# Performance work log

Hardware: AMD Instinct MI355X
Metric: run time of the kernel (lower is better)

The kernel has to match this reference:

```python
import jax, jax.numpy as jnp
import numpy as np

N = 8192        # particles
NBH = 64        # black holes
L = 46.0        # box side -> ~32 neighbors per particle at radius 4.5
K = 4           # kernel_size per axis
KK = K * K * K
EXTENT = 9.0    # radius_scale(1.5) * 6 * particle_radius(1)
EXTENT_BH = 4.0 * EXTENT
EP = 300000     # padded particle-particle edge count
EB = 160000     # padded bh->particle edge count
CIN = 4         # vel(3) + mass(1)
C0, C1, C2, C3 = 32, 64, 64, 3
FOUR_OVER_PI = 4.0 / np.pi


def _ball_query_np(query, points, radius, cap, pad_seg):
    """Brute-force host-side ball query. Returns padded (src, dst); padding
    uses dst == pad_seg (a sentinel segment that is dropped later)."""
    r2 = radius * radius
    src, dst = [], []
    for i in range(0, query.shape[0], 1024):
        q = query[i:i + 1024]
        d2 = ((q[:, None, :] - points[None, :, :]) ** 2).sum(-1)
        m = (d2 < r2) & (d2 > 0.0)  # radius_search_ignore_query_points
        qi, pj = np.nonzero(m)
        dst.append(qi + i)
        src.append(pj)
    src = np.concatenate(src).astype(np.int32)
    dst = np.concatenate(dst).astype(np.int32)
    n = min(len(src), cap)
    out_s = np.zeros(cap, np.int32)
    out_d = np.full(cap, pad_seg, np.int32)
    out_s[:n] = src[:n]
    out_d[:n] = dst[:n]
    return out_s, out_d


def setup_inputs() -> dict:
    rng = np.random.RandomState(0)
    pos = (rng.rand(N, 3) * L).astype(np.float32)
    vel = rng.randn(N, 3).astype(np.float32)
    mass = rng.rand(N).astype(np.float32)
    bh_pos = (rng.rand(NBH, 3) * L).astype(np.float32)
    bh_vel = rng.randn(NBH, 3).astype(np.float32)
    bh_mass = (rng.rand(NBH) * 10.0).astype(np.float32)
    pp_src, pp_dst = _ball_query_np(pos, pos, EXTENT * 0.5, EP, N)
    bh_src, bh_dst = _ball_query_np(pos, bh_pos, EXTENT_BH * 0.5, EB, N)

    def w(*s):
        return (rng.randn(*s) * 0.05).astype(np.float32)

    inp = dict(
        pos=jnp.asarray(pos), vel=jnp.asarray(vel), mass=jnp.asarray(mass),
        bh_pos=jnp.asarray(bh_pos), bh_vel=jnp.asarray(bh_vel), bh_mass=jnp.asarray(bh_mass),
        pp_src=jnp.asarray(pp_src), pp_dst=jnp.asarray(pp_dst),
        bh_src=jnp.asarray(bh_src), bh_dst=jnp.asarray(bh_dst),
        W0a=jnp.asarray(w(K, K, K, CIN, C0)), b0a=jnp.zeros(C0, jnp.float32),
        Wd0=jnp.asarray(w(CIN, C0)), bd0=jnp.zeros(C0, jnp.float32),
        W0b=jnp.asarray(w(K, K, K, CIN, C0)), b0b=jnp.zeros(C0, jnp.float32),
        W1=jnp.asarray(w(K, K, K, 3 * C0, C1)), b1=jnp.zeros(C1, jnp.float32),
        Wd1=jnp.asarray(w(3 * C0, C1)), bd1=jnp.zeros(C1, jnp.float32),
        W2=jnp.asarray(w(K, K, K, C1, C2)), b2=jnp.zeros(C2, jnp.float32),
        Wd2=jnp.asarray(w(C1, C2)), bd2=jnp.zeros(C2, jnp.float32),
        W3=jnp.asarray(w(K, K, K, C2, C3)), b3=jnp.zeros(C3, jnp.float32),
        Wd3=jnp.asarray(w(C2, C3)), bd3=jnp.zeros(C3, jnp.float32),
    )
    return inp


def _ball_to_cube(p):
    """Volume-preserving map from unit ball to cube [-1,1]^3 (sphere->cylinder->cube)."""
    eps = 1e-8
    x, y, z = p[..., 0], p[..., 1], p[..., 2]
    sq = x * x + y * y + z * z
    nrm = jnp.sqrt(sq)
    xy = x * x + y * y
    # sphere -> cylinder
    caps = 1.25 * z * z > xy
    s_caps = jnp.sqrt(3.0 * nrm / (nrm + jnp.abs(z) + eps))
    s_side = nrm / jnp.sqrt(xy + eps)
    s = jnp.where(caps, s_caps, s_side)
    valid = sq > eps
    cx = jnp.where(valid, x * s, 0.0)
    cy = jnp.where(valid, y * s, 0.0)
    cz = jnp.where(valid, jnp.where(caps, jnp.sign(z) * nrm, 1.5 * z), 0.0)
    # cylinder -> cube (concentric disc-to-square, area preserving)
    rxy = jnp.sqrt(cx * cx + cy * cy)
    regA = cx * cx >= cy * cy
    safe_cx = jnp.where(jnp.abs(cx) > eps, cx, 1.0)
    safe_cy = jnp.where(jnp.abs(cy) > eps, cy, 1.0)
    uA = jnp.sign(cx) * rxy
    vA = uA * FOUR_OVER_PI * jnp.arctan(cy / safe_cx)
    vB = jnp.sign(cy) * rxy
    uB = vB * FOUR_OVER_PI * jnp.arctan(cx / safe_cy)
    okxy = rxy > eps
    u = jnp.where(okxy, jnp.where(regA, uA, uB), 0.0)
    v = jnp.where(okxy, jnp.where(regA, vA, vB), 0.0)
    return jnp.stack([u, v, cz], axis=-1)


def _cconv(feats, pos_src, pos_dst, src, dst, W, b, extent):
    """ContinuousConv: ball-query edges (src->dst), poly6 window, trilinear
    kernel interpolation (align_corners=True), scatter-sum, no normalization."""
    n_out = pos_dst.shape[0]
    radius = 0.5 * extent
    ps = jnp.take(pos_src, src, axis=0)                       # [E,3]
    pd = jnp.take(pos_dst, jnp.minimum(dst, n_out - 1), axis=0)
    d = (ps - pd) * (1.0 / radius)                            # normalized offsets
    r_sqr = jnp.sum(d * d, axis=-1)
    win = jnp.clip((1.0 - r_sqr) ** 3, 0.0, 1.0)              # window_poly6
    u = _ball_to_cube(d)                                      # in [-1,1]^3
    t = (u + 1.0) * (0.5 * (K - 1))                           # align_corners grid coords
    i0f = jnp.clip(jnp.floor(t), 0, K - 2)
    i0 = i0f.astype(jnp.int32)
    f = t - i0f                                               # trilinear fractions
    fe = jnp.take(feats, src, axis=0) * win[:, None]          # [E,Cin]
    Cin = feats.shape[1]
    Wf = W.reshape(KK, Cin, -1)
    T = jnp.zeros(((n_out + 1) * KK, Cin), feats.dtype)
    for dx in (0, 1):
        wx = f[:, 0] if dx else 1.0 - f[:, 0]
        for dy in (0, 1):
            wy = f[:, 1] if dy else 1.0 - f[:, 1]
            for dz in (0, 1):
                wz = f[:, 2] if dz else 1.0 - f[:, 2]
                k = ((i0[:, 0] + dx) * K + (i0[:, 1] + dy)) * K + (i0[:, 2] + dz)
                idx = dst * KK + k                            # sentinel dst==n_out dropped
                T = T + jax.ops.segment_sum((wx * wy * wz)[:, None] * fe, idx,
                                            num_segments=(n_out + 1) * KK)
    T = T.reshape(n_out + 1, KK, Cin)[:n_out]                 # [N,64,Cin]
    return jnp.einsum('nkc,kcd->nd', T, Wf) + b


def _forward(pos, vel, mass, bh_pos, bh_vel, bh_mass,
             W0a, b0a, Wd0, bd0, W0b, b0b, W1, b1, Wd1, bd1,
             W2, b2, Wd2, bd2, W3, b3, Wd3, bd3,
             pp_src, pp_dst, bh_src, bh_dst):
    feats = jnp.concatenate([vel, mass[:, None]], axis=-1)        # [N,4]
    bh_feats = jnp.concatenate([bh_vel, bh_mass[:, None]], axis=-1)
    c0 = _cconv(feats, pos, pos, pp_src, pp_dst, W0a, b0a, EXTENT)      # [N,32]
    d0 = feats @ Wd0 + bd0                                               # [N,32]
    cb = _cconv(bh_feats, bh_pos, pos, bh_src, bh_dst, W0b, b0b, EXTENT_BH)
    h = jnp.concatenate([c0, cb, d0], axis=-1)                           # [N,96]
    c1 = jax.nn.relu(_cconv(h, pos, pos, pp_src, pp_dst, W1, b1, EXTENT))
    d1 = jax.nn.relu(h @ Wd1 + bd1)
    h1 = c1 + d1                                                         # 64 != 96 -> no residual
    c2 = jax.nn.relu(_cconv(h1, pos, pos, pp_src, pp_dst, W2, b2, EXTENT))
    d2 = jax.nn.relu(h1 @ Wd2 + bd2)
    h2 = c2 + d2 + h1                                                    # 64 == 64 -> residual
    c3 = _cconv(h2, pos, pos, pp_src, pp_dst, W3, b3, EXTENT)
    d3 = h2 @ Wd3 + bd3
    return c3 + d3                                                       # accelerations [N,3]


def reference(pos, vel, mass, bh_pos, bh_vel, bh_mass,
              pp_src, pp_dst, bh_src, bh_dst,
              W0a, b0a, Wd0, bd0, W0b, b0b, W1, b1, Wd1, bd1,
              W2, b2, Wd2, bd2, W3, b3, Wd3, bd3):
    return _forward(pos, vel, mass, bh_pos, bh_vel, bh_mass,
                    W0a, b0a, Wd0, bd0, W0b, b0b, W1, b1, Wd1, bd1,
                    W2, b2, Wd2, bd2, W3, b3, Wd3, bd3,
                    pp_src, pp_dst, bh_src, bh_dst)
```

## Files before the change

### kernel.cpp

```cpp
#include <hip/hip_runtime.h>
#include <math.h>

#define NPART 8192
#define NBHX  64
#define EPX   300000
#define EBX   160000
#define FOUR_OVER_PI 1.27323954473516f

typedef __attribute__((ext_vector_type(8))) short bf16x8;
typedef __attribute__((ext_vector_type(4))) float f32x4;

__device__ __forceinline__ float signf(float x){ return (x>0.f)?1.f:((x<0.f)?-1.f:0.f); }
__device__ __forceinline__ unsigned short f2bf(float f){
  unsigned u = __float_as_uint(f);
  u += 0x7FFFu + ((u >> 16) & 1u);
  return (unsigned short)(u >> 16);
}
__device__ __forceinline__ float bf2f(unsigned short h){
  return __uint_as_float(((unsigned)h) << 16);
}
__device__ __forceinline__ float bfl(unsigned u){ return __uint_as_float(u << 16); }
__device__ __forceinline__ float bfh(unsigned u){ return __uint_as_float(u & 0xffff0000u); }

__global__ void feats_kernel(const float* __restrict__ vel, const float* __restrict__ mass,
                             const float* __restrict__ bhvel, const float* __restrict__ bhmass,
                             float* __restrict__ feats, float* __restrict__ bhfeats,
                             int* __restrict__ hist) {
  int i = blockIdx.x*256 + threadIdx.x;
  if (i < NPART) {
    feats[i*4+0]=vel[i*3+0]; feats[i*4+1]=vel[i*3+1]; feats[i*4+2]=vel[i*3+2]; feats[i*4+3]=mass[i];
  }
  if (i < NBHX) {
    bhfeats[i*4+0]=bhvel[i*3+0]; bhfeats[i*4+1]=bhvel[i*3+1]; bhfeats[i*4+2]=bhvel[i*3+2]; bhfeats[i*4+3]=bhmass[i];
  }
  if (i < 4096) hist[i] = 0;
}

__global__ void geom_kernel(const float* __restrict__ ppos, const float* __restrict__ qpos,
                            const int* __restrict__ src, const int* __restrict__ dst,
                            int E, int n_out, float inv_radius,
                            int* __restrict__ gsb, float* __restrict__ gw) {
  int e = blockIdx.x*256 + threadIdx.x;
  if (e >= E) return;
  int s = src[e], t = dst[e];
  if (t >= n_out) {
    gsb[e] = s*64;
    for (int j=0;j<8;j++) gw[(size_t)e*8+j] = 0.f;
    return;
  }
  float x = (ppos[s*3+0] - qpos[t*3+0]) * inv_radius;
  float y = (ppos[s*3+1] - qpos[t*3+1]) * inv_radius;
  float z = (ppos[s*3+2] - qpos[t*3+2]) * inv_radius;
  float r2 = x*x + y*y + z*z;
  float w1 = 1.f - r2;
  float win = fminf(fmaxf(w1*w1*w1, 0.f), 1.f);
  const float eps = 1e-8f;
  float nrm = sqrtf(r2);
  float xy = x*x + y*y;
  bool caps = (1.25f*z*z > xy);
  float s_caps = sqrtf(3.f*nrm/(nrm + fabsf(z) + eps));
  float s_side = nrm / sqrtf(xy + eps);
  float sc = caps ? s_caps : s_side;
  bool valid = r2 > eps;
  float cx = valid ? x*sc : 0.f;
  float cy = valid ? y*sc : 0.f;
  float cz = valid ? (caps ? signf(z)*nrm : 1.5f*z) : 0.f;
  float rxy = sqrtf(cx*cx + cy*cy);
  bool regA = (cx*cx >= cy*cy);
  float safe_cx = (fabsf(cx) > eps) ? cx : 1.0f;
  float safe_cy = (fabsf(cy) > eps) ? cy : 1.0f;
  float uA = signf(cx)*rxy;
  float vA = uA * FOUR_OVER_PI * atanf(cy/safe_cx);
  float vB = signf(cy)*rxy;
  float uB = vB * FOUR_OVER_PI * atanf(cx/safe_cy);
  bool okxy = rxy > eps;
  float u = okxy ? (regA ? uA : uB) : 0.f;
  float v = okxy ? (regA ? vA : vB) : 0.f;
  float tt[3] = { (u+1.f)*1.5f, (v+1.f)*1.5f, (cz+1.f)*1.5f };
  int i0[3]; float f[3];
#pragma unroll
  for (int ax=0; ax<3; ax++) {
    float tf = floorf(tt[ax]);
    tf = fminf(fmaxf(tf, 0.f), 2.f);
    i0[ax] = (int)tf;
    f[ax] = tt[ax] - tf;
  }
  gsb[e] = s*64 + ((i0[0]*4 + i0[1])*4 + i0[2]);
#pragma unroll
  for (int j=0;j<8;j++) {
    float wx = (j&4) ? f[0] : 1.f - f[0];
    float wy = (j&2) ? f[1] : 1.f - f[1];
    float wz = (j&1) ? f[2] : 1.f - f[2];
    gw[(size_t)e*8+j] = win * wx * wy * wz;
  }
}

__global__ void csr2_kernel(const int* __restrict__ dstP, const int* __restrict__ dstB,
                            int* __restrict__ rsP, int* __restrict__ rsB) {
  int i = blockIdx.x*256 + threadIdx.x;
  if (i <= NPART) {
    int lo = 0, hi = EPX;
    while (lo < hi) { int mid = (lo+hi)>>1; if (dstP[mid] < i) lo = mid+1; else hi = mid; }
    rsP[i] = lo;
  }
  int k = i - (NPART+1);
  if (k >= 0 && k <= NPART) {
    int lo = 0, hi = EBX;
    while (lo < hi) { int mid = (lo+hi)>>1; if (dstB[mid] < k) lo = mid+1; else hi = mid; }
    rsB[k] = lo;
  }
}

__global__ void cellhist_kernel(const float* __restrict__ pos, int* __restrict__ cell,
                                int* __restrict__ hist) {
  int i = blockIdx.x*256 + threadIdx.x;
  if (i >= NPART) return;
  const float inv = 16.0f/46.0f;
  int ix = min(15, max(0, (int)(pos[i*3+0]*inv)));
  int iy = min(15, max(0, (int)(pos[i*3+1]*inv)));
  int iz = min(15, max(0, (int)(pos[i*3+2]*inv)));
  int c = (ix*16+iy)*16+iz;
  cell[i] = c;
  atomicAdd(&hist[c], 1);
}
__global__ __launch_bounds__(256) void scan_kernel(const int* __restrict__ hist, int* __restrict__ offs) {
  __shared__ int wsum[4];
  int t = threadIdx.x;
  int base = t*16;
  int loc[16]; int s = 0;
#pragma unroll
  for (int i=0;i<16;i++){ loc[i]=s; s+=hist[base+i]; }
  int lane = t & 63, wv = t >> 6;
  int pre = s;
  for (int off=1; off<64; off<<=1) {
    int v = __shfl_up(pre, off);
    if (lane >= off) pre += v;
  }
  if (lane == 63) wsum[wv] = pre;
  __syncthreads();
  int wbase = 0;
  for (int w=0; w<wv; w++) wbase += wsum[w];
  int ex = wbase + pre - s;
#pragma unroll
  for (int i=0;i<16;i++) offs[base+i] = ex + loc[i];
}
__global__ void scatterorder_kernel(const int* __restrict__ cell, int* __restrict__ offs,
                                    int* __restrict__ order) {
  int i = blockIdx.x*256 + threadIdx.x;
  if (i >= NPART) return;
  int p = atomicAdd(&offs[cell[i]], 1);
  order[p] = i;
}

__device__ __forceinline__ int swz_block(int bid, int nb) {
  return (bid & 7)*(nb >> 3) + (bid >> 3);
}

__global__ void wtrans3_kernel(const float* __restrict__ W1, const float* __restrict__ W2,
                               const float* __restrict__ W3,
                               unsigned short* __restrict__ BT1, unsigned short* __restrict__ BT2,
                               unsigned short* __restrict__ BT3) {
  int idx = blockIdx.x*256 + threadIdx.x;
  const int S1 = 4096*96, S2 = 4096*64, S3 = 256*64;
  if (idx < S1) {
    int n = idx/96, c = idx - n*96; int k = n>>6, d = n&63;
    BT1[idx] = f2bf(W1[((size_t)k*96 + c)*64 + d]);
  } else if (idx < S1+S2) {
    int t = idx - S1; int n = t>>6, c = t&63; int k = n>>6, d = n&63;
    BT2[t] = f2bf(W2[((size_t)k*64 + c)*64 + d]);
  } else if (idx < S1+S2+S3) {
    int t = idx - S1 - S2; int n = t>>6, c = t&63; int k = n>>2, d = n&3;
    BT3[t] = f2bf((d < 3) ? W3[((size_t)k*64 + c)*3 + d] : 0.f);
  }
}

__global__ void y0_kernel(const float* __restrict__ feats4, const float* __restrict__ bhfeats,
                          const float* __restrict__ W0a, const float* __restrict__ W0b,
                          unsigned short* __restrict__ Y0a, unsigned short* __restrict__ Y0b) {
  int idx = blockIdx.x*256 + threadIdx.x;
  if (idx >= (NPART+NBHX)*256) return;
  int oct = idx & 3, k = (idx>>2) & 63, s = idx >> 8;
  bool bh = (s >= NPART);
  int sl = bh ? s - NPART : s;
  const float* fp = (bh ? bhfeats : feats4) + (size_t)sl*4;
  const float* W0 = bh ? W0b : W0a;
  unsigned short* Y = (bh ? Y0b : Y0a) + ((size_t)sl*64 + k)*32 + oct*8;
  float4 f = *(const float4*)fp;
  const float* w = W0 + (size_t)k*128 + oct*8;
  unsigned short o[8];
#pragma unroll
  for (int i=0;i<8;i++) {
    float v = f.x*w[i] + f.y*w[32+i] + f.z*w[64+i] + f.w*w[96+i];
    o[i] = f2bf(v);
  }
  uint4 u;
  u.x = (unsigned)o[0] | ((unsigned)o[1]<<16);
  u.y = (unsigned)o[2] | ((unsigned)o[3]<<16);
  u.z = (unsigned)o[4] | ((unsigned)o[5]<<16);
  u.w = (unsigned)o[6] | ((unsigned)o[7]<<16);
  *(uint4*)Y = u;
}

__global__ __launch_bounds__(256) void gemm_y_kernel(
    const unsigned short* __restrict__ A, const unsigned short* __restrict__ BT,
    int KC, int Ntot, unsigned short* __restrict__ Y) {
  const int wid  = threadIdx.x >> 6;
  const int lane = threadIdx.x & 63;
  const int r = lane & 15, g = lane >> 4;
  const int m0 = blockIdx.x*128 + wid*32;
  const int n0 = blockIdx.y*64;
  f32x4 acc[2][4];
#pragma unroll
  for (int h=0;h<2;h++)
#pragma unroll
    for (int n=0;n<4;n++) acc[h][n] = (f32x4){0.f,0.f,0.f,0.f};
  const unsigned short* A0 = A + (size_t)(m0 + r)*KC;
  const unsigned short* A1 = A + (size_t)(m0 + 16 + r)*KC;
  for (int k0 = 0; k0 < KC; k0 += 32) {
    int ko = k0 + g*8;
    bf16x8 a0 = *(const bf16x8*)(A0 + ko);
    bf16x8 a1 = *(const bf16x8*)(A1 + ko);
#pragma unroll
    for (int n=0; n<4; n++) {
      bf16x8 b = *(const bf16x8*)(BT + (size_t)(n0 + n*16 + r)*KC + ko);
      acc[0][n] = __builtin_amdgcn_mfma_f32_16x16x32_bf16(a0, b, acc[0][n], 0, 0, 0);
      acc[1][n] = __builtin_amdgcn_mfma_f32_16x16x32_bf16(a1, b, acc[1][n], 0, 0, 0);
    }
  }
#pragma unroll
  for (int h=0;h<2;h++)
#pragma unroll
    for (int n=0;n<4;n++)
#pragma unroll
      for (int j=0;j<4;j++)
        Y[(size_t)(m0 + h*16 + g*4 + j)*Ntot + n0 + n*16 + r] = f2bf(acc[h][n][j]);
}

__device__ __forceinline__ void xor_add4(f32x4& a, int mask) {
  a.x += __shfl_xor(a.x, mask);
  a.y += __shfl_xor(a.y, mask);
  a.z += __shfl_xor(a.z, mask);
  a.w += __shfl_xor(a.w, mask);
}

__global__ __launch_bounds__(256) void gather_l0_kernel(
    const int* __restrict__ order,
    const int* __restrict__ rsP, const int* __restrict__ gsbP, const float* __restrict__ gwP,
    const int* __restrict__ rsB, const int* __restrict__ gsbB, const float* __restrict__ gwB,
    const unsigned short* __restrict__ Y0a, const unsigned short* __restrict__ Y0b,
    const float* __restrict__ feats4, const float* __restrict__ Wd0, const float* __restrict__ bd0,
    const float* __restrict__ b0a, const float* __restrict__ b0b,
    float* __restrict__ hf, unsigned short* __restrict__ hb) {
  const int sw = swz_block(blockIdx.x, gridDim.x);
  const int node = order[sw*4 + (threadIdx.x >> 6)];
  const int lane = threadIdx.x & 63;
  const int j = lane >> 3, cg = lane & 7;
  const int koff = ((j&4)<<2) | ((j&2)<<1) | (j&1);
  f32x4 accP = {0.f,0.f,0.f,0.f}, accB = {0.f,0.f,0.f,0.f};
  {
    int e0 = rsP[node], e1 = rsP[node+1];
    int e = e0;
    for (; e + 4 <= e1; e += 4) {
      uint2 y[4]; float w[4];
#pragma unroll
      for (int i=0;i<4;i++) {
        int sb = gsbP[e+i];
        y[i] = *(const uint2*)(Y0a + ((size_t)(sb + koff))*32 + cg*4);
        w[i] = gwP[(size_t)(e+i)*8 + j];
      }
#pragma unroll
      for (int i=0;i<4;i++) {
        accP.x += w[i]*bfl(y[i].x); accP.y += w[i]*bfh(y[i].x);
        accP.z += w[i]*bfl(y[i].y); accP.w += w[i]*bfh(y[i].y);
      }
    }
    for (; e < e1; e++) {
      int sb = gsbP[e];
      uint2 y = *(const uint2*)(Y0a + ((size_t)(sb + koff))*32 + cg*4);
      float w = gwP[(size_t)e*8 + j];
      accP.x += w*bfl(y.x); accP.y += w*bfh(y.x);
      accP.z += w*bfl(y.y); accP.w += w*bfh(y.y);
    }
  }
  {
    int e0 = rsB[node], e1 = rsB[node+1];
    int e = e0;
    for (; e + 4 <= e1; e += 4) {
      uint2 y[4]; float w[4];
#pragma unroll
      for (int i=0;i<4;i++) {
        int sb = gsbB[e+i];
        y[i] = *(const uint2*)(Y0b + ((size_t)(sb + koff))*32 + cg*4);
        w[i] = gwB[(size_t)(e+i)*8 + j];
      }
#pragma unroll
      for (int i=0;i<4;i++) {
        accB.x += w[i]*bfl(y[i].x); accB.y += w[i]*bfh(y[i].x);
        accB.z += w[i]*bfl(y[i].y); accB.w += w[i]*bfh(y[i].y);
      }
    }
    for (; e < e1; e++) {
      int sb = gsbB[e];
      uint2 y = *(const uint2*)(Y0b + ((size_t)(sb + koff))*32 + cg*4);
      float w = gwB[(size_t)e*8 + j];
      accB.x += w*bfl(y.x); accB.y += w*bfh(y.x);
      accB.z += w*bfl(y.y); accB.w += w*bfh(y.y);
    }
  }
  xor_add4(accP, 8);  xor_add4(accP, 16); xor_add4(accP, 32);
  xor_add4(accB, 8);  xor_add4(accB, 16); xor_add4(accB, 32);
  if (lane < 8) {
    float4 f = *(const float4*)(feats4 + (size_t)node*4);
    float4 ba = *(const float4*)(b0a + cg*4);
    float4 bb = *(const float4*)(b0b + cg*4);
    float4 bdv = *(const float4*)(bd0 + cg*4);
    float4 w0v = *(const float4*)(Wd0 + 0*32 + cg*4);
    float4 w1v = *(const float4*)(Wd0 + 1*32 + cg*4);
    float4 w2v = *(const float4*)(Wd0 + 2*32 + cg*4);
    float4 w3v = *(const float4*)(Wd0 + 3*32 + cg*4);
    float4 dd;
    dd.x = bdv.x + f.x*w0v.x + f.y*w1v.x + f.z*w2v.x + f.w*w3v.x;
    dd.y = bdv.y + f.x*w0v.y + f.y*w1v.y + f.z*w2v.y + f.w*w3v.y;
    dd.z = bdv.z + f.x*w0v.z + f.y*w1v.z + f.z*w2v.z + f.w*w3v.z;
    dd.w = bdv.w + f.x*w0v.w + f.y*w1v.w + f.z*w2v.w + f.w*w3v.w;
    float4 c0; c0.x = accP.x + ba.x; c0.y = accP.y + ba.y; c0.z = accP.z + ba.z; c0.w = accP.w + ba.w;
    float4 cb; cb.x = accB.x + bb.x; cb.y = accB.y + bb.y; cb.z = accB.z + bb.z; cb.w = accB.w + bb.w;
    size_t o = (size_t)node*96;
    *(float4*)(hf + o + cg*4)      = c0;
    *(float4*)(hf + o + 32 + cg*4) = cb;
    *(float4*)(hf + o + 64 + cg*4) = dd;
    ushort4 u0 = {f2bf(c0.x), f2bf(c0.y), f2bf(c0.z), f2bf(c0.w)};
    ushort4 u1 = {f2bf(cb.x), f2bf(cb.y), f2bf(cb.z), f2bf(cb.w)};
    ushort4 u2 = {f2bf(dd.x), f2bf(dd.y), f2bf(dd.z), f2bf(dd.w)};
    *(ushort4*)(hb + o + cg*4)      = u0;
    *(ushort4*)(hb + o + 32 + cg*4) = u1;
    *(ushort4*)(hb + o + 64 + cg*4) = u2;
  }
}

template<int DCIN, bool ADDSKIP>
__global__ __launch_bounds__(128) void gather64_kernel(
    const int* __restrict__ order,
    const int* __restrict__ rs, const int* __restrict__ gsb, const float* __restrict__ gw,
    const unsigned short* __restrict__ Y,
    const float* __restrict__ Xf, const float* __restrict__ Wd, const float* __restrict__ bd,
    const float* __restrict__ bconv, const float* __restrict__ skip,
    float* __restrict__ outf, unsigned short* __restrict__ outb) {
  const int sw = swz_block(blockIdx.x, gridDim.x);
  const int node = order[sw];
  const int wave = threadIdx.x >> 6;
  const int lane = threadIdx.x & 63;
  const int j = lane >> 3, cg = lane & 7;
  const int koff = ((j&4)<<2) | ((j&2)<<1) | (j&1);
  __shared__ __align__(16) float red[64*8];
  f32x4 accA = {0.f,0.f,0.f,0.f}, accB = {0.f,0.f,0.f,0.f};
  const int e0 = rs[node], e1 = rs[node+1];
  int e = e0 + wave;
  for (; e + 6 < e1; e += 8) {
    uint4 y[4]; float w[4];
#pragma unroll
    for (int i=0;i<4;i++) {
      int ee = e + i*2;
      int sb = gsb[ee];
      y[i] = *(const uint4*)(Y + ((size_t)(sb + koff))*64 + cg*8);
      w[i] = gw[(size_t)ee*8 + j];
    }
#pragma unroll
    for (int i=0;i<4;i++) {
      accA.x += w[i]*bfl(y[i].x); accA.y += w[i]*bfh(y[i].x);
      accA.z += w[i]*bfl(y[i].y); accA.w += w[i]*bfh(y[i].y);
      accB.x += w[i]*bfl(y[i].z); accB.y += w[i]*bfh(y[i].z);
      accB.z += w[i]*bfl(y[i].w); accB.w += w[i]*bfh(y[i].w);
    }
  }
  for (; e < e1; e += 2) {
    int sb = gsb[e];
    uint4 y = *(const uint4*)(Y + ((size_t)(sb + koff))*64 + cg*8);
    float w = gw[(size_t)e*8 + j];
    accA.x += w*bfl(y.x); accA.y += w*bfh(y.x);
    accA.z += w*bfl(y.y); accA.w += w*bfh(y.y);
    accB.x += w*bfl(y.z); accB.y += w*bfh(y.z);
    accB.z += w*bfl(y.w); accB.w += w*bfh(y.w);
  }
  if (wave == 1) {
    *(f32x4*)(red + lane*8)     = accA;
    *(f32x4*)(red + lane*8 + 4) = accB;
  }
  __syncthreads();
  if (wave == 0) {
    {
      f32x4 oA = *(const f32x4*)(red + lane*8);
      f32x4 oB = *(const f32x4*)(red + lane*8 + 4);
      accA.x += oA.x; accA.y += oA.y; accA.z += oA.z; accA.w += oA.w;
      accB.x += oB.x; accB.y += oB.y; accB.z += oB.z; accB.w += oB.w;
    }
    constexpr int KQ = DCIN/8;
    f32x4 ddA = {0.f,0.f,0.f,0.f}, ddB = {0.f,0.f,0.f,0.f};
    const float* x = Xf + (size_t)node*DCIN + j*KQ;
#pragma unroll
    for (int kk=0; kk<KQ; kk++) {
      float xv = x[kk];
      float4 w0 = *(const float4*)(Wd + (size_t)(j*KQ+kk)*64 + cg*8);
      float4 w1 = *(const float4*)(Wd + (size_t)(j*KQ+kk)*64 + cg*8 + 4);
      ddA.x += xv*w0.x; ddA.y += xv*w0.y; ddA.z += xv*w0.z; ddA.w += xv*w0.w;
      ddB.x += xv*w1.x; ddB.y += xv*w1.y; ddB.z += xv*w1.z; ddB.w += xv*w1.w;
    }
    xor_add4(accA, 8); xor_add4(accA, 16); xor_add4(accA, 32);
    xor_add4(accB, 8); xor_add4(accB, 16); xor_add4(accB, 32);
    xor_add4(ddA, 8);  xor_add4(ddA, 16);  xor_add4(ddA, 32);
    xor_add4(ddB, 8);  xor_add4(ddB, 16);  xor_add4(ddB, 32);
    if (lane < 8) {
      float4 bc0 = *(const float4*)(bconv + cg*8);
      float4 bc1 = *(const float4*)(bconv + cg*8 + 4);
      float4 bd0v = *(const float4*)(bd + cg*8);
      float4 bd1v = *(const float4*)(bd + cg*8 + 4);
      float4 v0, v1;
      v0.x = fmaxf(accA.x + bc0.x, 0.f) + fmaxf(ddA.x + bd0v.x, 0.f);
      v0.y = fmaxf(accA.y + bc0.y, 0.f) + fmaxf(ddA.y + bd0v.y, 0.f);
      v0.z = fmaxf(accA.z + bc0.z, 0.f) + fmaxf(ddA.z + bd0v.z, 0.f);
      v0.w = fmaxf(accA.w + bc0.w, 0.f) + fmaxf(ddA.w + bd0v.w, 0.f);
      v1.x = fmaxf(accB.x + bc1.x, 0.f) + fmaxf(ddB.x + bd1v.x, 0.f);
      v1.y = fmaxf(accB.y + bc1.y, 0.f) + fmaxf(ddB.y + bd1v.y, 0.f);
      v1.z = fmaxf(accB.z + bc1.z, 0.f) + fmaxf(ddB.z + bd1v.z, 0.f);
      v1.w = fmaxf(accB.w + bc1.w, 0.f) + fmaxf(ddB.w + bd1v.w, 0.f);
      if (ADDSKIP) {
        float4 s0 = *(const float4*)(skip + (size_t)node*64 + cg*8);
        float4 s1 = *(const float4*)(skip + (size_t)node*64 + cg*8 + 4);
        v0.x += s0.x; v0.y += s0.y; v0.z += s0.z; v0.w += s0.w;
        v1.x += s1.x; v1.y += s1.y; v1.z += s1.z; v1.w += s1.w;
      }
      *(float4*)(outf + (size_t)node*64 + cg*8)     = v0;
      *(float4*)(outf + (size_t)node*64 + cg*8 + 4) = v1;
      ushort4 u0 = {f2bf(v0.x), f2bf(v0.y), f2bf(v0.z), f2bf(v0.w)};
      ushort4 u1 = {f2bf(v1.x), f2bf(v1.y), f2bf(v1.z), f2bf(v1.w)};
      *(ushort4*)(outb + (size_t)node*64 + cg*8)     = u0;
      *(ushort4*)(outb + (size_t)node*64 + cg*8 + 4) = u1;
    }
  }
}

__global__ __launch_bounds__(256) void gather3_kernel(
    const int* __restrict__ order,
    const int* __restrict__ rs, const int* __restrict__ gsb, const float* __restrict__ gw,
    const unsigned short* __restrict__ Y3,
    const float* __restrict__ h2f, const float* __restrict__ Wd3, const float* __restrict__ bd3,
    const float* __restrict__ b3, float* __restrict__ out) {
  const int sw = swz_block(blockIdx.x, gridDim.x);
  const int node = order[sw*4 + (threadIdx.x >> 6)];
  const int lane = threadIdx.x & 63;
  const int e2 = lane >> 5, j = (lane >> 2) & 7, dd = lane & 3;
  const int koff = ((j&4)<<2)|((j&2)<<1)|(j&1);
  float acc = 0.f;
  const int e0 = rs[node], e1 = rs[node+1];
  for (int e = e0; e < e1; e += 2) {
    int ee = e + e2;
    bool v = ee < e1;
    int ix = v ? ee : e;
    int sb = gsb[ix];
    float w = v ? gw[(size_t)ix*8 + j] : 0.f;
    acc += w * bf2f(Y3[((size_t)(sb + koff))*4 + dd]);
  }
  acc += __shfl_xor(acc, 4);
  acc += __shfl_xor(acc, 8);
  acc += __shfl_xor(acc, 16);
  acc += __shfl_down(acc, 32);
  if (lane < 3) {
    float d3 = bd3[lane];
    const float* x = h2f + (size_t)node*64;
#pragma unroll 8
    for (int c=0;c<64;c++) d3 += x[c]*Wd3[c*3 + lane];
    out[(size_t)node*3 + lane] = acc + b3[lane] + d3;
  }
}

extern "C" void kernel_launch(void* const* d_in, const int* in_sizes, int n_in,
                              void* d_out, int out_size, void* d_ws, size_t ws_size,
                              hipStream_t stream) {
  const float* pos    = (const float*)d_in[0];
  const float* vel    = (const float*)d_in[1];
  const float* mass   = (const float*)d_in[2];
  const float* bh_pos = (const float*)d_in[3];
  const float* bh_vel = (const float*)d_in[4];
  const float* bh_mass= (const float*)d_in[5];
  const int* pp_src   = (const int*)d_in[6];
  const int* pp_dst   = (const int*)d_in[7];
  const int* bh_src   = (const int*)d_in[8];
  const int* bh_dst   = (const int*)d_in[9];
  const float* W0a=(const float*)d_in[10]; const float* b0a=(const float*)d_in[11];
  const float* Wd0=(const float*)d_in[12]; const float* bd0=(const float*)d_in[13];
  const float* W0b=(const float*)d_in[14]; const float* b0b=(const float*)d_in[15];
  const float* W1 =(const float*)d_in[16]; const float* b1 =(const float*)d_in[17];
  const float* Wd1=(const float*)d_in[18]; const float* bd1=(const float*)d_in[19];
  const float* W2 =(const float*)d_in[20]; const float* b2 =(const float*)d_in[21];
  const float* Wd2=(const float*)d_in[22]; const float* bd2=(const float*)d_in[23];
  const float* W3 =(const float*)d_in[24]; const float* b3 =(const float*)d_in[25];
  const float* Wd3=(const float*)d_in[26]; const float* bd3=(const float*)d_in[27];
  float* out = (float*)d_out;
  char* wsb = (char*)d_ws;

  size_t off = 0;
  auto alloc = [&](size_t nbytes){ size_t o = off; off += (nbytes + 255) & ~((size_t)255); return o; };
  size_t feats_o   = alloc((size_t)NPART*4*4);
  size_t bhfeats_o = alloc((size_t)NBHX*4*4);
  size_t rs_pp_o   = alloc(8256*4);
  size_t rs_bh_o   = alloc(8256*4);
  size_t gsb_pp_o  = alloc((size_t)EPX*4);
  size_t gw_pp_o   = alloc((size_t)EPX*8*4);
  size_t gsb_bh_o  = alloc((size_t)EBX*4);
  size_t gw_bh_o   = alloc((size_t)EBX*8*4);
  size_t hf_o  = alloc((size_t)NPART*96*4);
  size_t hb_o  = alloc((size_t)NPART*96*2);
  size_t h1f_o = alloc((size_t)NPART*64*4);
  size_t h1b_o = alloc((size_t)NPART*64*2);
  size_t h2f_o = alloc((size_t)NPART*64*4);
  size_t h2b_o = alloc((size_t)NPART*64*2);
  size_t bt1_o = alloc((size_t)4096*96*2);
  size_t bt2_o = alloc((size_t)4096*64*2);
  size_t bt3_o = alloc((size_t)256*64*2);
  size_t y0b_o = alloc((size_t)NBHX*64*32*2);
  size_t cell_o = alloc((size_t)NPART*4);
  size_t hist_o = alloc((size_t)4096*4);
  size_t order_o= alloc((size_t)NPART*4);
  size_t y_o   = alloc((size_t)NPART*4096*2);

  float* featsP = (float*)(wsb + feats_o); float* bhfeatsP = (float*)(wsb + bhfeats_o);
  int* rsPP = (int*)(wsb + rs_pp_o); int* rsBH = (int*)(wsb + rs_bh_o);
  int* gsbP = (int*)(wsb + gsb_pp_o); float* gwP = (float*)(wsb + gw_pp_o);
  int* gsbB = (int*)(wsb + gsb_bh_o); float* gwB = (float*)(wsb + gw_bh_o);
  float* hf  = (float*)(wsb + hf_o);  unsigned short* hb  = (unsigned short*)(wsb + hb_o);
  float* h1f = (float*)(wsb + h1f_o); unsigned short* h1b = (unsigned short*)(wsb + h1b_o);
  float* h2f = (float*)(wsb + h2f_o); unsigned short* h2b = (unsigned short*)(wsb + h2b_o);
  unsigned short* BT1 = (unsigned short*)(wsb + bt1_o);
  unsigned short* BT2 = (unsigned short*)(wsb + bt2_o);
  unsigned short* BT3 = (unsigned short*)(wsb + bt3_o);
  unsigned short* Y0b = (unsigned short*)(wsb + y0b_o);
  int* cellA = (int*)(wsb + cell_o);
  int* histA = (int*)(wsb + hist_o);
  int* orderA= (int*)(wsb + order_o);
  unsigned short* Ybuf = (unsigned short*)(wsb + y_o);

  feats_kernel<<<(NPART+255)/256, 256, 0, stream>>>(vel, mass, bh_vel, bh_mass, featsP, bhfeatsP, histA);
  geom_kernel<<<(EPX+255)/256, 256, 0, stream>>>(pos, pos, pp_src, pp_dst, EPX, NPART, 1.f/4.5f, gsbP, gwP);
  geom_kernel<<<(EBX+255)/256, 256, 0, stream>>>(bh_pos, pos, bh_src, bh_dst, EBX, NPART, 1.f/18.f, gsbB, gwB);
  csr2_kernel<<<(2*(NPART+1)+255)/256, 256, 0, stream>>>(pp_dst, bh_dst, rsPP, rsBH);
  cellhist_kernel<<<NPART/256, 256, 0, stream>>>(pos, cellA, histA);
  scan_kernel<<<1, 256, 0, stream>>>(histA, histA);
  scatterorder_kernel<<<NPART/256, 256, 0, stream>>>(cellA, histA, orderA);
  wtrans3_kernel<<<(4096*96 + 4096*64 + 256*64 + 255)/256, 256, 0, stream>>>(W1, W2, W3, BT1, BT2, BT3);

  y0_kernel<<<((NPART+NBHX)*256+255)/256, 256, 0, stream>>>(featsP, bhfeatsP, W0a, W0b, Ybuf, Y0b);
  gather_l0_kernel<<<NPART/4, 256, 0, stream>>>(orderA, rsPP, gsbP, gwP, rsBH, gsbB, gwB,
                                                Ybuf, Y0b, featsP, Wd0, bd0, b0a, b0b, hf, hb);
  {
    dim3 g(NPART/128, 4096/64);
    gemm_y_kernel<<<g, 256, 0, stream>>>(hb, BT1, 96, 4096, Ybuf);
    gather64_kernel<96,false><<<NPART, 128, 0, stream>>>(orderA, rsPP, gsbP, gwP, Ybuf,
        hf, Wd1, bd1, b1, nullptr, h1f, h1b);
  }
  {
    dim3 g(NPART/128, 4096/64);
    gemm_y_kernel<<<g, 256, 0, stream>>>(h1b, BT2, 64, 4096, Ybuf);
    gather64_kernel<64,true><<<NPART, 128, 0, stream>>>(orderA, rsPP, gsbP, gwP, Ybuf,
        h1f, Wd2, bd2, b2, h1f, h2f, h2b);
  }
  {
    dim3 g(NPART/128, 256/64);
    gemm_y_kernel<<<g, 256, 0, stream>>>(h2b, BT3, 64, 256, Ybuf);
    gather3_kernel<<<NPART/4, 256, 0, stream>>>(orderA, rsPP, gsbP, gwP, Ybuf,
        h2f, Wd3, bd3, b3, out);
  }
}
```

Before: 214.8 us.

## Pack per-corner edge index and weight together, merge prep kernels, split dense work

Stores each edge's base index alongside each of its 8 trilinear weights as a uint2 record, so gather kernels fetch index and weight in one load instead of two dependent loads. Merges the geometry kernels for particle and black-hole edges into one launch, folds feature packing into the CSR kernel and cell histogram into the weight transpose kernel. In gather64, the dense-layer dot product is split across both waves and reduced through shared memory. The cost is duplicating the index eight times, which roughly doubles the geometry output bytes, plus a larger shared reduction buffer.

```diff
diff --git a/kernel.cpp b/kernel.cpp
--- a/kernel.cpp
+++ b/kernel.cpp
@@ -22,35 +22,30 @@
 __device__ __forceinline__ float bfl(unsigned u){ return __uint_as_float(u << 16); }
 __device__ __forceinline__ float bfh(unsigned u){ return __uint_as_float(u & 0xffff0000u); }
 
-__global__ void feats_kernel(const float* __restrict__ vel, const float* __restrict__ mass,
-                             const float* __restrict__ bhvel, const float* __restrict__ bhmass,
-                             float* __restrict__ feats, float* __restrict__ bhfeats,
+__global__ void geom2_kernel(const float* __restrict__ pos, const float* __restrict__ bh_pos,
+                             const int* __restrict__ srcP, const int* __restrict__ dstP,
+                             const int* __restrict__ srcB, const int* __restrict__ dstB,
+                             uint2* __restrict__ gewP, uint2* __restrict__ gewB,
                              int* __restrict__ hist) {
-  int i = blockIdx.x*256 + threadIdx.x;
-  if (i < NPART) {
-    feats[i*4+0]=vel[i*3+0]; feats[i*4+1]=vel[i*3+1]; feats[i*4+2]=vel[i*3+2]; feats[i*4+3]=mass[i];
-  }
-  if (i < NBHX) {
-    bhfeats[i*4+0]=bhvel[i*3+0]; bhfeats[i*4+1]=bhvel[i*3+1]; bhfeats[i*4+2]=bhvel[i*3+2]; bhfeats[i*4+3]=bhmass[i];
-  }
-  if (i < 4096) hist[i] = 0;
-}
-
-__global__ void geom_kernel(const float* __restrict__ ppos, const float* __restrict__ qpos,
-                            const int* __restrict__ src, const int* __restrict__ dst,
-                            int E, int n_out, float inv_radius,
-                            int* __restrict__ gsb, float* __restrict__ gw) {
-  int e = blockIdx.x*256 + threadIdx.x;
-  if (e >= E) return;
+  int idx = blockIdx.x*256 + threadIdx.x;
+  if (idx < 4096) hist[idx] = 0;
+  bool isP = idx < EPX;
+  int e = isP ? idx : idx - EPX;
+  if (!isP && e >= EBX) return;
+  const int* src = isP ? srcP : srcB;
+  const int* dst = isP ? dstP : dstB;
+  const float* ppos = isP ? pos : bh_pos;
+  uint2* gew = isP ? gewP : gewB;
+  float inv_radius = isP ? (1.f/4.5f) : (1.f/18.f);
   int s = src[e], t = dst[e];
-  if (t >= n_out) {
-    gsb[e] = s*64;
-    for (int j=0;j<8;j++) gw[(size_t)e*8+j] = 0.f;
+  if (t >= NPART) {
+    uint2 z; z.x = s*64; z.y = 0;
+    for (int j=0;j<8;j++) gew[(size_t)e*8+j] = z;
     return;
   }
-  float x = (ppos[s*3+0] - qpos[t*3+0]) * inv_radius;
-  float y = (ppos[s*3+1] - qpos[t*3+1]) * inv_radius;
-  float z = (ppos[s*3+2] - qpos[t*3+2]) * inv_radius;
+  float x = (ppos[s*3+0] - pos[t*3+0]) * inv_radius;
+  float y = (ppos[s*3+1] - pos[t*3+1]) * inv_radius;
+  float z = (ppos[s*3+2] - pos[t*3+2]) * inv_radius;
   float r2 = x*x + y*y + z*z;
   float w1 = 1.f - r2;
   float win = fminf(fmaxf(w1*w1*w1, 0.f), 1.f);
@@ -85,19 +80,29 @@
     i0[ax] = (int)tf;
     f[ax] = tt[ax] - tf;
   }
-  gsb[e] = s*64 + ((i0[0]*4 + i0[1])*4 + i0[2]);
+  unsigned sb = s*64 + ((i0[0]*4 + i0[1])*4 + i0[2]);
 #pragma unroll
   for (int j=0;j<8;j++) {
     float wx = (j&4) ? f[0] : 1.f - f[0];
     float wy = (j&2) ? f[1] : 1.f - f[1];
     float wz = (j&1) ? f[2] : 1.f - f[2];
-    gw[(size_t)e*8+j] = win * wx * wy * wz;
-  }
-}
-
-__global__ void csr2_kernel(const int* __restrict__ dstP, const int* __restrict__ dstB,
+    uint2 o; o.x = sb; o.y = __float_as_uint(win * wx * wy * wz);
+    gew[(size_t)e*8+j] = o;
+  }
+}
+
+__global__ void prep_kernel(const float* __restrict__ vel, const float* __restrict__ mass,
+                            const float* __restrict__ bhvel, const float* __restrict__ bhmass,
+                            float* __restrict__ feats, float* __restrict__ bhfeats,
+                            const int* __restrict__ dstP, const int* __restrict__ dstB,
                             int* __restrict__ rsP, int* __restrict__ rsB) {
   int i = blockIdx.x*256 + threadIdx.x;
+  if (i < NPART) {
+    feats[i*4+0]=vel[i*3+0]; feats[i*4+1]=vel[i*3+1]; feats[i*4+2]=vel[i*3+2]; feats[i*4+3]=mass[i];
+  }
+  if (i < NBHX) {
+    bhfeats[i*4+0]=bhvel[i*3+0]; bhfeats[i*4+1]=bhvel[i*3+1]; bhfeats[i*4+2]=bhvel[i*3+2]; bhfeats[i*4+3]=bhmass[i];
+  }
   if (i <= NPART) {
     int lo = 0, hi = EPX;
     while (lo < hi) { int mid = (lo+hi)>>1; if (dstP[mid] < i) lo = mid+1; else hi = mid; }
@@ -111,56 +116,25 @@
   }
 }
 
-__global__ void cellhist_kernel(const float* __restrict__ pos, int* __restrict__ cell,
-                                int* __restrict__ hist) {
-  int i = blockIdx.x*256 + threadIdx.x;
-  if (i >= NPART) return;
-  const float inv = 16.0f/46.0f;
-  int ix = min(15, max(0, (int)(pos[i*3+0]*inv)));
-  int iy = min(15, max(0, (int)(pos[i*3+1]*inv)));
-  int iz = min(15, max(0, (int)(pos[i*3+2]*inv)));
-  int c = (ix*16+iy)*16+iz;
-  cell[i] = c;
-  atomicAdd(&hist[c], 1);
-}
-__global__ __launch_bounds__(256) void scan_kernel(const int* __restrict__ hist, int* __restrict__ offs) {
-  __shared__ int wsum[4];
-  int t = threadIdx.x;
-  int base = t*16;
-  int loc[16]; int s = 0;
-#pragma unroll
-  for (int i=0;i<16;i++){ loc[i]=s; s+=hist[base+i]; }
-  int lane = t & 63, wv = t >> 6;
-  int pre = s;
-  for (int off=1; off<64; off<<=1) {
-    int v = __shfl_up(pre, off);
-    if (lane >= off) pre += v;
-  }
-  if (lane == 63) wsum[wv] = pre;
-  __syncthreads();
-  int wbase = 0;
-  for (int w=0; w<wv; w++) wbase += wsum[w];
-  int ex = wbase + pre - s;
-#pragma unroll
-  for (int i=0;i<16;i++) offs[base+i] = ex + loc[i];
-}
-__global__ void scatterorder_kernel(const int* __restrict__ cell, int* __restrict__ offs,
-                                    int* __restrict__ order) {
-  int i = blockIdx.x*256 + threadIdx.x;
-  if (i >= NPART) return;
-  int p = atomicAdd(&offs[cell[i]], 1);
-  order[p] = i;
-}
-
-__device__ __forceinline__ int swz_block(int bid, int nb) {
-  return (bid & 7)*(nb >> 3) + (bid >> 3);
-}
-
-__global__ void wtrans3_kernel(const float* __restrict__ W1, const float* __restrict__ W2,
-                               const float* __restrict__ W3,
-                               unsigned short* __restrict__ BT1, unsigned short* __restrict__ BT2,
-                               unsigned short* __restrict__ BT3) {
-  int idx = blockIdx.x*256 + threadIdx.x;
+__global__ void cellw_kernel(const float* __restrict__ pos, int* __restrict__ cell,
+                             int* __restrict__ hist,
+                             const float* __restrict__ W1, const float* __restrict__ W2,
+                             const float* __restrict__ W3,
+                             unsigned short* __restrict__ BT1, unsigned short* __restrict__ BT2,
+                             unsigned short* __restrict__ BT3) {
+  int b = blockIdx.x;
+  if (b < 32) {
+    int i = b*256 + threadIdx.x;
+    const float inv = 16.0f/46.0f;
+    int ix = min(15, max(0, (int)(pos[i*3+0]*inv)));
+    int iy = min(15, max(0, (int)(pos[i*3+1]*inv)));
+    int iz = min(15, max(0, (int)(pos[i*3+2]*inv)));
+    int c = (ix*16+iy)*16+iz;
+    cell[i] = c;
+    atomicAdd(&hist[c], 1);
+    return;
+  }
+  int idx = (b-32)*256 + threadIdx.x;
   const int S1 = 4096*96, S2 = 4096*64, S3 = 256*64;
   if (idx < S1) {
     int n = idx/96, c = idx - n*96; int k = n>>6, d = n&63;
@@ -172,6 +146,39 @@
     int t = idx - S1 - S2; int n = t>>6, c = t&63; int k = n>>2, d = n&3;
     BT3[t] = f2bf((d < 3) ? W3[((size_t)k*64 + c)*3 + d] : 0.f);
   }
+}
+
+__global__ __launch_bounds__(256) void scan_kernel(const int* __restrict__ hist, int* __restrict__ offs) {
+  __shared__ int wsum[4];
+  int t = threadIdx.x;
+  int base = t*16;
+  int loc[16]; int s = 0;
+#pragma unroll
+  for (int i=0;i<16;i++){ loc[i]=s; s+=hist[base+i]; }
+  int lane = t & 63, wv = t >> 6;
+  int pre = s;
+  for (int off=1; off<64; off<<=1) {
+    int v = __shfl_up(pre, off);
+    if (lane >= off) pre += v;
+  }
+  if (lane == 63) wsum[wv] = pre;
+  __syncthreads();
+  int wbase = 0;
+  for (int w=0; w<wv; w++) wbase += wsum[w];
+  int ex = wbase + pre - s;
+#pragma unroll
+  for (int i=0;i<16;i++) offs[base+i] = ex + loc[i];
+}
+__global__ void scatterorder_kernel(const int* __restrict__ cell, int* __restrict__ offs,
+                                    int* __restrict__ order) {
+  int i = blockIdx.x*256 + threadIdx.x;
+  if (i >= NPART) return;
+  int p = atomicAdd(&offs[cell[i]], 1);
+  order[p] = i;
+}
+
+__device__ __forceinline__ int swz_block(int bid, int nb) {
+  return (bid & 7)*(nb >> 3) + (bid >> 3);
 }
 
 __global__ void y0_kernel(const float* __restrict__ feats4, const float* __restrict__ bhfeats,
@@ -245,8 +252,8 @@
 
 __global__ __launch_bounds__(256) void gather_l0_kernel(
     const int* __restrict__ order,
-    const int* __restrict__ rsP, const int* __restrict__ gsbP, const float* __restrict__ gwP,
-    const int* __restrict__ rsB, const int* __restrict__ gsbB, const float* __restrict__ gwB,
+    const int* __restrict__ rsP, const uint2* __restrict__ gewP,
+    const int* __restrict__ rsB, const uint2* __restrict__ gewB,
     const unsigned short* __restrict__ Y0a, const unsigned short* __restrict__ Y0b,
     const float* __restrict__ feats4, const float* __restrict__ Wd0, const float* __restrict__ bd0,
     const float* __restrict__ b0a, const float* __restrict__ b0b,
@@ -261,23 +268,22 @@
     int e0 = rsP[node], e1 = rsP[node+1];
     int e = e0;
     for (; e + 4 <= e1; e += 4) {
-      uint2 y[4]; float w[4];
+      uint2 p[4]; uint2 y[4];
+#pragma unroll
+      for (int i=0;i<4;i++) p[i] = gewP[(size_t)(e+i)*8 + j];
+#pragma unroll
+      for (int i=0;i<4;i++) y[i] = *(const uint2*)(Y0a + ((size_t)(p[i].x + koff))*32 + cg*4);
 #pragma unroll
       for (int i=0;i<4;i++) {
-        int sb = gsbP[e+i];
-        y[i] = *(const uint2*)(Y0a + ((size_t)(sb + koff))*32 + cg*4);
-        w[i] = gwP[(size_t)(e+i)*8 + j];
+        float w = __uint_as_float(p[i].y);
+        accP.x += w*bfl(y[i].x); accP.y += w*bfh(y[i].x);
+        accP.z += w*bfl(y[i].y); accP.w += w*bfh(y[i].y);
       }
-#pragma unroll
-      for (int i=0;i<4;i++) {
-        accP.x += w[i]*bfl(y[i].x); accP.y += w[i]*bfh(y[i].x);
-        accP.z += w[i]*bfl(y[i].y); accP.w += w[i]*bfh(y[i].y);
-      }
     }
     for (; e < e1; e++) {
-      int sb = gsbP[e];
-      uint2 y = *(const uint2*)(Y0a + ((size_t)(sb + koff))*32 + cg*4);
-      float w = gwP[(size_t)e*8 + j];
+      uint2 p = gewP[(size_t)e*8 + j];
+      uint2 y = *(const uint2*)(Y0a + ((size_t)(p.x + koff))*32 + cg*4);
+      float w = __uint_as_float(p.y);
       accP.x += w*bfl(y.x); accP.y += w*bfh(y.x);
       accP.z += w*bfl(y.y); accP.w += w*bfh(y.y);
     }
@@ -286,23 +292,22 @@
     int e0 = rsB[node], e1 = rsB[node+1];
     int e = e0;
     for (; e + 4 <= e1; e += 4) {
-      uint2 y[4]; float w[4];
+      uint2 p[4]; uint2 y[4];
+#pragma unroll
+      for (int i=0;i<4;i++) p[i] = gewB[(size_t)(e+i)*8 + j];
+#pragma unroll
+      for (int i=0;i<4;i++) y[i] = *(const uint2*)(Y0b + ((size_t)(p[i].x + koff))*32 + cg*4);
 #pragma unroll
       for (int i=0;i<4;i++) {
-        int sb = gsbB[e+i];
-        y[i] = *(const uint2*)(Y0b + ((size_t)(sb + koff))*32 + cg*4);
-        w[i] = gwB[(size_t)(e+i)*8 + j];
+        float w = __uint_as_float(p[i].y);
+        accB.x += w*bfl(y[i].x); accB.y += w*bfh(y[i].x);
+        accB.z += w*bfl(y[i].y); accB.w += w*bfh(y[i].y);
       }
-#pragma unroll
-      for (int i=0;i<4;i++) {
-        accB.x += w[i]*bfl(y[i].x); accB.y += w[i]*bfh(y[i].x);
-        accB.z += w[i]*bfl(y[i].y); accB.w += w[i]*bfh(y[i].y);
-      }
     }
     for (; e < e1; e++) {
-      int sb = gsbB[e];
-      uint2 y = *(const uint2*)(Y0b + ((size_t)(sb + koff))*32 + cg*4);
-      float w = gwB[(size_t)e*8 + j];
+      uint2 p = gewB[(size_t)e*8 + j];
+      uint2 y = *(const uint2*)(Y0b + ((size_t)(p.x + koff))*32 + cg*4);
+      float w = __uint_as_float(p.y);
       accB.x += w*bfl(y.x); accB.y += w*bfh(y.x);
       accB.z += w*bfl(y.y); accB.w += w*bfh(y.y);
     }
@@ -341,7 +346,7 @@
 template<int DCIN, bool ADDSKIP>
 __global__ __launch_bounds__(128) void gather64_kernel(
     const int* __restrict__ order,
-    const int* __restrict__ rs, const int* __restrict__ gsb, const float* __restrict__ gw,
+    const int* __restrict__ rs, const uint2* __restrict__ gew,
     const unsigned short* __restrict__ Y,
     const float* __restrict__ Xf, const float* __restrict__ Wd, const float* __restrict__ bd,
     const float* __restrict__ bconv, const float* __restrict__ skip,
@@ -352,58 +357,65 @@
   const int lane = threadIdx.x & 63;
   const int j = lane >> 3, cg = lane & 7;
   const int koff = ((j&4)<<2) | ((j&2)<<1) | (j&1);
-  __shared__ __align__(16) float red[64*8];
+  __shared__ __align__(16) float red[64*16];
   f32x4 accA = {0.f,0.f,0.f,0.f}, accB = {0.f,0.f,0.f,0.f};
   const int e0 = rs[node], e1 = rs[node+1];
   int e = e0 + wave;
   for (; e + 6 < e1; e += 8) {
-    uint4 y[4]; float w[4];
+    uint2 p[4]; uint4 y[4];
+#pragma unroll
+    for (int i=0;i<4;i++) p[i] = gew[(size_t)(e + i*2)*8 + j];
+#pragma unroll
+    for (int i=0;i<4;i++) y[i] = *(const uint4*)(Y + ((size_t)(p[i].x + koff))*64 + cg*8);
 #pragma unroll
     for (int i=0;i<4;i++) {
-      int ee = e + i*2;
-      int sb = gsb[ee];
-      y[i] = *(const uint4*)(Y + ((size_t)(sb + koff))*64 + cg*8);
-      w[i] = gw[(size_t)ee*8 + j];
-    }
-#pragma unroll
-    for (int i=0;i<4;i++) {
-      accA.x += w[i]*bfl(y[i].x); accA.y += w[i]*bfh(y[i].x);
-      accA.z += w[i]*bfl(y[i].y); accA.w += w[i]*bfh(y[i].y);
-      accB.x += w[i]*bfl(y[i].z); accB.y += w[i]*bfh(y[i].z);
-      accB.z += w[i]*bfl(y[i].w); accB.w += w[i]*bfh(y[i].w);
+      float w = __uint_as_float(p[i].y);
+      accA.x += w*bfl(y[i].x); accA.y += w*bfh(y[i].x);
+      accA.z += w*bfl(y[i].y); accA.w += w*bfh(y[i].y);
+      accB.x += w*bfl(y[i].z); accB.y += w*bfh(y[i].z);
+      accB.z += w*bfl(y[i].w); accB.w += w*bfh(y[i].w);
     }
   }
   for (; e < e1; e += 2) {
-    int sb = gsb[e];
-    uint4 y = *(const uint4*)(Y + ((size_t)(sb + koff))*64 + cg*8);
-    float w = gw[(size_t)e*8 + j];
+    uint2 p = gew[(size_t)e*8 + j];
+    uint4 y = *(const uint4*)(Y + ((size_t)(p.x + koff))*64 + cg*8);
+    float w = __uint_as_float(p.y);
     accA.x += w*bfl(y.x); accA.y += w*bfh(y.x);
     accA.z += w*bfl(y.y); accA.w += w*bfh(y.y);
     accB.x += w*bfl(y.z); accB.y += w*bfh(y.z);
     accB.z += w*bfl(y.w); accB.w += w*bfh(y.w);
   }
+  constexpr int KQ = DCIN/16;
+  f32x4 ddA = {0.f,0.f,0.f,0.f}, ddB = {0.f,0.f,0.f,0.f};
+  {
+    const int seg = wave*8 + j;
+    const float* x = Xf + (size_t)node*DCIN + seg*KQ;
+#pragma unroll
+    for (int kk=0; kk<KQ; kk++) {
+      float xv = x[kk];
+      float4 w0 = *(const float4*)(Wd + (size_t)(seg*KQ+kk)*64 + cg*8);
+      float4 w1 = *(const float4*)(Wd + (size_t)(seg*KQ+kk)*64 + cg*8 + 4);
+      ddA.x += xv*w0.x; ddA.y += xv*w0.y; ddA.z += xv*w0.z; ddA.w += xv*w0.w;
+      ddB.x += xv*w1.x; ddB.y += xv*w1.y; ddB.z += xv*w1.z; ddB.w += xv*w1.w;
+    }
+  }
   if (wave == 1) {
-    *(f32x4*)(red + lane*8)     = accA;
-    *(f32x4*)(red + lane*8 + 4) = accB;
+    *(f32x4*)(red + lane*16)      = accA;
+    *(f32x4*)(red + lane*16 + 4)  = accB;
+    *(f32x4*)(red + lane*16 + 8)  = ddA;
+    *(f32x4*)(red + lane*16 + 12) = ddB;
   }
   __syncthreads();
   if (wave == 0) {
     {
-      f32x4 oA = *(const f32x4*)(red + lane*8);
-      f32x4 oB = *(const f32x4*)(red + lane*8 + 4);
+      f32x4 oA = *(const f32x4*)(red + lane*16);
+      f32x4 oB = *(const f32x4*)(red + lane*16 + 4);
+      f32x4 oC = *(const f32x4*)(red + lane*16 + 8);
+      f32x4 oD = *(const f32x4*)(red + lane*16 + 12);
       accA.x += oA.x; accA.y += oA.y; accA.z += oA.z; accA.w += oA.w;
       accB.x += oB.x; accB.y += oB.y; accB.z += oB.z; accB.w += oB.w;
-    }
-    constexpr int KQ = DCIN/8;
-    f32x4 ddA = {0.f,0.f,0.f,0.f}, ddB = {0.f,0.f,0.f,0.f};
-    const float* x = Xf + (size_t)node*DCIN + j*KQ;
-#pragma unroll
-    for (int kk=0; kk<KQ; kk++) {
-      float xv = x[kk];
-      float4 w0 = *(const float4*)(Wd + (size_t)(j*KQ+kk)*64 + cg*8);
-      float4 w1 = *(const float4*)(Wd + (size_t)(j*KQ+kk)*64 + cg*8 + 4);
-      ddA.x += xv*w0.x; ddA.y += xv*w0.y; ddA.z += xv*w0.z; ddA.w += xv*w0.w;
-      ddB.x += xv*w1.x; ddB.y += xv*w1.y; ddB.z += xv*w1.z; ddB.w += xv*w1.w;
+      ddA.x += oC.x; ddA.y += oC.y; ddA.z += oC.z; ddA.w += oC.w;
+      ddB.x += oD.x; ddB.y += oD.y; ddB.z += oD.z; ddB.w += oD.w;
     }
     xor_add4(accA, 8); xor_add4(accA, 16); xor_add4(accA, 32);
     xor_add4(accB, 8); xor_add4(accB, 16); xor_add4(accB, 32);
@@ -441,7 +453,7 @@
 
 __global__ __launch_bounds__(256) void gather3_kernel(
     const int* __restrict__ order,
-    const int* __restrict__ rs, const int* __restrict__ gsb, const float* __restrict__ gw,
+    const int* __restrict__ rs, const uint2* __restrict__ gew,
     const unsigned short* __restrict__ Y3,
     const float* __restrict__ h2f, const float* __restrict__ Wd3, const float* __restrict__ bd3,
     const float* __restrict__ b3, float* __restrict__ out) {
@@ -456,9 +468,9 @@
     int ee = e + e2;
     bool v = ee < e1;
     int ix = v ? ee : e;
-    int sb = gsb[ix];
-    float w = v ? gw[(size_t)ix*8 + j] : 0.f;
-    acc += w * bf2f(Y3[((size_t)(sb + koff))*4 + dd]);
+    uint2 p = gew[(size_t)ix*8 + j];
+    float w = v ? __uint_as_float(p.y) : 0.f;
+    acc += w * bf2f(Y3[((size_t)(p.x + koff))*4 + dd]);
   }
   acc += __shfl_xor(acc, 4);
   acc += __shfl_xor(acc, 8);
@@ -504,10 +516,8 @@
   size_t bhfeats_o = alloc((size_t)NBHX*4*4);
   size_t rs_pp_o   = alloc(8256*4);
   size_t rs_bh_o   = alloc(8256*4);
-  size_t gsb_pp_o  = alloc((size_t)EPX*4);
-  size_t gw_pp_o   = alloc((size_t)EPX*8*4);
-  size_t gsb_bh_o  = alloc((size_t)EBX*4);
-  size_t gw_bh_o   = alloc((size_t)EBX*8*4);
+  size_t gew_pp_o  = alloc((size_t)EPX*8*8);
+  size_t gew_bh_o  = alloc((size_t)EBX*8*8);
   size_t hf_o  = alloc((size_t)NPART*96*4);
   size_t hb_o  = alloc((size_t)NPART*96*2);
   size_t h1f_o = alloc((size_t)NPART*64*4);
@@ -525,8 +535,8 @@
 
   float* featsP = (float*)(wsb + feats_o); float* bhfeatsP = (float*)(wsb + bhfeats_o);
   int* rsPP = (int*)(wsb + rs_pp_o); int* rsBH = (int*)(wsb + rs_bh_o);
-  int* gsbP = (int*)(wsb + gsb_pp_o); float* gwP = (float*)(wsb + gw_pp_o);
-  int* gsbB = (int*)(wsb + gsb_bh_o); float* gwB = (float*)(wsb + gw_bh_o);
+  uint2* gewP = (uint2*)(wsb + gew_pp_o);
+  uint2* gewB = (uint2*)(wsb + gew_bh_o);
   float* hf  = (float*)(wsb + hf_o);  unsigned short* hb  = (unsigned short*)(wsb + hb_o);
   float* h1f = (float*)(wsb + h1f_o); unsigned short* h1b = (unsigned short*)(wsb + h1b_o);
   float* h2f = (float*)(wsb + h2f_o); unsigned short* h2b = (unsigned short*)(wsb + h2b_o);
@@ -539,34 +549,34 @@
   int* orderA= (int*)(wsb + order_o);
   unsigned short* Ybuf = (unsigned short*)(wsb + y_o);
 
-  feats_kernel<<<(NPART+255)/256, 256, 0, stream>>>(vel, mass, bh_vel, bh_mass, featsP, bhfeatsP, histA);
-  geom_kernel<<<(EPX+255)/256, 256, 0, stream>>>(pos, pos, pp_src, pp_dst, EPX, NPART, 1.f/4.5f, gsbP, gwP);
-  geom_kernel<<<(EBX+255)/256, 256, 0, stream>>>(bh_pos, pos, bh_src, bh_dst, EBX, NPART, 1.f/18.f, gsbB, gwB);
-  csr2_kernel<<<(2*(NPART+1)+255)/256, 256, 0, stream>>>(pp_dst, bh_dst, rsPP, rsBH);
-  cellhist_kernel<<<NPART/256, 256, 0, stream>>>(pos, cellA, histA);
+  geom2_kernel<<<(EPX+EBX+255)/256, 256, 0, stream>>>(pos, bh_pos, pp_src, pp_dst, bh_src, bh_dst,
+                                                      gewP, gewB, histA);
+  prep_kernel<<<(2*(NPART+1)+255)/256, 256, 0, stream>>>(vel, mass, bh_vel, bh_mass,
+                                                         featsP, bhfeatsP, pp_dst, bh_dst, rsPP, rsBH);
+  cellw_kernel<<<32 + (4096*96 + 4096*64 + 256*64 + 255)/256, 256, 0, stream>>>(
+      pos, cellA, histA, W1, W2, W3, BT1, BT2, BT3);
   scan_kernel<<<1, 256, 0, stream>>>(histA, histA);
   scatterorder_kernel<<<NPART/256, 256, 0, stream>>>(cellA, histA, orderA);
-  wtrans3_kernel<<<(4096*96 + 4096*64 + 256*64 + 255)/256, 256, 0, stream>>>(W1, W2, W3, BT1, BT2, BT3);
 
   y0_kernel<<<((NPART+NBHX)*256+255)/256, 256, 0, stream>>>(featsP, bhfeatsP, W0a, W0b, Ybuf, Y0b);
-  gather_l0_kernel<<<NPART/4, 256, 0, stream>>>(orderA, rsPP, gsbP, gwP, rsBH, gsbB, gwB,
+  gather_l0_kernel<<<NPART/4, 256, 0, stream>>>(orderA, rsPP, gewP, rsBH, gewB,
                                                 Ybuf, Y0b, featsP, Wd0, bd0, b0a, b0b, hf, hb);
   {
     dim3 g(NPART/128, 4096/64);
     gemm_y_kernel<<<g, 256, 0, stream>>>(hb, BT1, 96, 4096, Ybuf);
-    gather64_kernel<96,false><<<NPART, 128, 0, stream>>>(orderA, rsPP, gsbP, gwP, Ybuf,
+    gather64_kernel<96,false><<<NPART, 128, 0, stream>>>(orderA, rsPP, gewP, Ybuf,
         hf, Wd1, bd1, b1, nullptr, h1f, h1b);
   }
   {
     dim3 g(NPART/128, 4096/64);
     gemm_y_kernel<<<g, 256, 0, stream>>>(h1b, BT2, 64, 4096, Ybuf);
-    gather64_kernel<64,true><<<NPART, 128, 0, stream>>>(orderA, rsPP, gsbP, gwP, Ybuf,
+    gather64_kernel<64,true><<<NPART, 128, 0, stream>>>(orderA, rsPP, gewP, Ybuf,
         h1f, Wd2, bd2, b2, h1f, h2f, h2b);
   }
   {
     dim3 g(NPART/128, 256/64);
     gemm_y_kernel<<<g, 256, 0, stream>>>(h2b, BT3, 64, 256, Ybuf);
-    gather3_kernel<<<NPART/4, 256, 0, stream>>>(orderA, rsPP, gsbP, gwP, Ybuf,
+    gather3_kernel<<<NPART/4, 256, 0, stream>>>(orderA, rsPP, gewP, Ybuf,
         h2f, Wd3, bd3, b3, out);
   }
 }
```

New measurement: 219.6 us. +2.2%, slower.
